# Kernel optimization log

Measured on AMD Instinct MI355X. Metric: run time of the kernel, lower is better.

The kernel has to match this reference:

```python
import jax, jax.numpy as jnp
import numpy as np

L, B, S, D, H, FF = 6, 4, 1024, 256, 8, 128
DH = D // H
EPS = 1e-5


def _ln(x, w, b):
    m = x.mean(-1, keepdims=True)
    v = ((x - m) ** 2).mean(-1, keepdims=True)
    return (x - m) / jnp.sqrt(v + EPS) * w + b


def setup_inputs() -> dict:
    key = jax.random.key(0)
    ks = jax.random.split(key, 6)
    s = lambda k, shape: jax.random.normal(k, shape, jnp.float32) * 0.02
    return {
        "x": jax.random.normal(ks[0], (B, S, D), jnp.float32),
        "ln1_w": jnp.ones((L, D), jnp.float32),
        "ln1_b": jnp.zeros((L, D), jnp.float32),
        "wqkv": s(ks[1], (L, D, 3 * D)),   # qkv_linear, bias=False
        "wout": s(ks[2], (L, D, D)),       # out_linear, bias=False
        "ln2_w": jnp.ones((L, D), jnp.float32),
        "ln2_b": jnp.zeros((L, D), jnp.float32),
        "w1": s(ks[3], (L, D, 2 * FF)),    # Linear(d_model, 2*ff)
        "b1": jnp.zeros((L, 2 * FF), jnp.float32),
        "w2": s(ks[4], (L, FF, D)),        # Linear(ff, d_model)
        "b2": jnp.zeros((L, D), jnp.float32),
    }


def reference(x, ln1_w, ln1_b, wqkv, wout, ln2_w, ln2_b, w1, b1, w2, b2):
    attn_weights_list = []
    scale = 1.0 / jnp.sqrt(jnp.float32(DH))
    for i in range(L):
        # --- pre-norm multi-head attention ---
        xn = _ln(x, ln1_w[i], ln1_b[i])
        qkv = xn @ wqkv[i]                       # [B,S,3D]
        q, k, v = jnp.split(qkv, 3, axis=-1)
        rs = lambda t: t.reshape(B, S, H, DH).transpose(0, 2, 1, 3)  # b h s d
        q, k, v = rs(q), rs(k), rs(v)
        logits = jnp.einsum('bhid,bhjd->bhij', q, k) * scale
        aw = jax.nn.softmax(logits, axis=-1)     # [B,H,S,S] (dropout=0, eval)
        attn_weights_list.append(aw)
        o = jnp.einsum('bhij,bhjd->bhid', aw, v)
        o = o.transpose(0, 2, 1, 3).reshape(B, S, D) @ wout[i]
        x = x + o
        # --- pre-norm GEGLU FFN ---
        h = _ln(x, ln2_w[i], ln2_b[i]) @ w1[i] + b1[i]   # [B,S,2*FF]
        a, g = jnp.split(h, 2, axis=-1)
        x = x + (a * jax.nn.gelu(g, approximate=False)) @ w2[i] + b2[i]
    return x, jnp.stack(attn_weights_list)      # [B,S,D], [L,B,H,S,S]
```

## Files before the change

### kernel.cpp

```cpp
#include <hip/hip_runtime.h>
#include <hip/hip_bf16.h>

typedef __bf16 bf16x8 __attribute__((ext_vector_type(8)));
typedef __bf16 bf16x4 __attribute__((ext_vector_type(4)));
typedef __bf16 bf16x2 __attribute__((ext_vector_type(2)));
typedef float  f32x4  __attribute__((ext_vector_type(4)));

#define LAYERS 6
#define BATCH  4
#define SEQ    1024
#define DMODEL 256
#define NHEAD  8
#define DHEAD  32
#define FFDIM  128
#define ROWS   (BATCH*SEQ)
#define QKVN   (3*DMODEL)
#define QSCALE 0.2550348616f

static __device__ __forceinline__ bf16x8 ldg8(const __bf16* p) {
  return *reinterpret_cast<const bf16x8*>(p);
}
#define MFMA16(a, b, c) __builtin_amdgcn_mfma_f32_16x16x32_bf16((a), (b), (c), 0, 0, 0)

__global__ void k_prep(const float* __restrict__ wqkv, const float* __restrict__ wout,
                       const float* __restrict__ w1, const float* __restrict__ w2,
                       __bf16* __restrict__ wqkvT, __bf16* __restrict__ woutT,
                       __bf16* __restrict__ w1T, __bf16* __restrict__ w2T) {
  const int N1 = LAYERS * DMODEL * QKVN;
  const int N2 = LAYERS * DMODEL * DMODEL;
  const int N3 = LAYERS * DMODEL * 2 * FFDIM;
  const int N4 = LAYERS * FFDIM * DMODEL;
  int total = N1 + N2 + N3 + N4;
  for (int i = blockIdx.x * blockDim.x + threadIdx.x; i < total; i += gridDim.x * blockDim.x) {
    int j = i;
    if (j < N1) {
      int l = j / (DMODEL * QKVN), rc = j - l * (DMODEL * QKVN);
      int r = rc / QKVN, c = rc - r * QKVN;
      wqkvT[(size_t)l * DMODEL * QKVN + (size_t)c * DMODEL + r] = (__bf16)wqkv[j]; continue;
    } j -= N1;
    if (j < N2) {
      int l = j / (DMODEL * DMODEL), rc = j - l * (DMODEL * DMODEL);
      int r = rc / DMODEL, c = rc - r * DMODEL;
      woutT[(size_t)l * DMODEL * DMODEL + (size_t)c * DMODEL + r] = (__bf16)wout[j]; continue;
    } j -= N2;
    if (j < N3) {
      int l = j / (DMODEL * 2 * FFDIM), rc = j - l * (DMODEL * 2 * FFDIM);
      int r = rc / (2 * FFDIM), c = rc - r * (2 * FFDIM);
      w1T[(size_t)l * DMODEL * 2 * FFDIM + (size_t)c * DMODEL + r] = (__bf16)w1[j]; continue;
    } j -= N3;
    {
      int l = j / (FFDIM * DMODEL), rc = j - l * (FFDIM * DMODEL);
      int r = rc / DMODEL, c = rc - r * DMODEL;
      w2T[(size_t)l * FFDIM * DMODEL + (size_t)c * FFDIM + r] = (__bf16)w2[j];
    }
  }
}

__global__ __launch_bounds__(64) void k_ln(const float* __restrict__ x,
                                           const float* __restrict__ w,
                                           const float* __restrict__ b,
                                           __bf16* __restrict__ out) {
  int row = blockIdx.x, l = threadIdx.x;
  const float* xr = x + (size_t)row * DMODEL;
  float v[4];
  #pragma unroll
  for (int j = 0; j < 4; ++j) v[j] = xr[l + 64 * j];
  float s = v[0] + v[1] + v[2] + v[3];
  #pragma unroll
  for (int off = 32; off >= 1; off >>= 1) s += __shfl_xor(s, off);
  float mean = s * (1.0f / DMODEL);
  float sq = 0.f;
  #pragma unroll
  for (int j = 0; j < 4; ++j) { v[j] -= mean; sq += v[j] * v[j]; }
  #pragma unroll
  for (int off = 32; off >= 1; off >>= 1) sq += __shfl_xor(sq, off);
  float rstd = rsqrtf(sq * (1.0f / DMODEL) + 1e-5f);
  __bf16* orow = out + (size_t)row * DMODEL;
  #pragma unroll
  for (int j = 0; j < 4; ++j) {
    int c = l + 64 * j;
    orow[c] = (__bf16)(v[j] * rstd * w[c] + b[c]);
  }
}

__global__ __launch_bounds__(256) void k_qkv(const __bf16* __restrict__ xn,
                                             const __bf16* __restrict__ Bt,
                                             __bf16* __restrict__ qb,
                                             __bf16* __restrict__ kt,
                                             __bf16* __restrict__ vt) {
  int w = threadIdx.x >> 6, l = threadIdx.x & 63, lr = l & 15, lg = l >> 4;
  int m0 = blockIdx.x * 64 + w * 16;
  int n0 = blockIdx.y * 64;
  f32x4 acc[4] = {};
  const __bf16* ap = xn + (size_t)(m0 + lr) * DMODEL + 8 * lg;
  const __bf16* bp = Bt + (size_t)(n0 + lr) * DMODEL + 8 * lg;
  for (int kc = 0; kc < DMODEL; kc += 32) {
    bf16x8 a = ldg8(ap + kc);
    #pragma unroll
    for (int t = 0; t < 4; ++t) {
      bf16x8 b = ldg8(bp + (size_t)t * 16 * DMODEL + kc);
      acc[t] = MFMA16(a, b, acc[t]);
    }
  }
  int row = m0 + lg * 4;
  if (n0 < DMODEL) {
    #pragma unroll
    for (int t = 0; t < 4; ++t) {
      int col = n0 + t * 16 + lr;
      #pragma unroll
      for (int r = 0; r < 4; ++r)
        qb[(size_t)(row + r) * DMODEL + col] = (__bf16)(acc[t][r] * QSCALE);
    }
  } else if (n0 < 2 * DMODEL) {
    int b_ = row >> 10, s = row & (SEQ - 1);
    #pragma unroll
    for (int t = 0; t < 4; ++t) {
      int hdh = n0 - DMODEL + t * 16 + lr;
      int h = hdh >> 5, dh = hdh & 31;
      size_t base = ((size_t)(b_ * NHEAD + h) * SEQ + s) * DHEAD + dh;
      #pragma unroll
      for (int r = 0; r < 4; ++r) kt[base + (size_t)r * DHEAD] = (__bf16)acc[t][r];
    }
  } else {
    int b_ = row >> 10, s = row & (SEQ - 1);
    #pragma unroll
    for (int t = 0; t < 4; ++t) {
      int hdh = n0 - 2 * DMODEL + t * 16 + lr;
      int h = hdh >> 5, dh = hdh & 31;
      bf16x4 v4;
      #pragma unroll
      for (int r = 0; r < 4; ++r) v4[r] = (__bf16)acc[t][r];
      *reinterpret_cast<bf16x4*>(vt + ((size_t)(b_ * NHEAD + h) * DHEAD + dh) * SEQ + s) = v4;
    }
  }
}

__global__ __launch_bounds__(256, 4) void k_attn(const __bf16* __restrict__ qb,
                                                 const __bf16* __restrict__ kt,
                                                 const __bf16* __restrict__ vt,
                                                 __bf16* __restrict__ ob,
                                                 float* __restrict__ aw) {
  __shared__ __bf16 P[4][2][16][40];
  __shared__ float  Ssum[4][16];
  __shared__ float  OS[4][16][34];
  int h = blockIdx.y, b = blockIdx.z;
  int w = threadIdx.x >> 6, l = threadIdx.x & 63, lr = l & 15, lg = l >> 4;
  int q0 = blockIdx.x * 16;
  bf16x8 qf = ldg8(qb + ((size_t)(b * SEQ) + q0 + lr) * DMODEL + h * DHEAD + 8 * lg);
  const __bf16* ktb = kt + (size_t)(b * NHEAD + h) * SEQ * DHEAD + 8 * lg;
  const __bf16* vtb = vt + (size_t)(b * NHEAD + h) * DHEAD * SEQ;
  f32x4 z = {};
  int kbeg = w * 256;

  f32x4 p[16];
  f32x4 accO[2] = {};

  #pragma unroll
  for (int j = 0; j < 8; ++j) {
    int kc = kbeg + j * 32;
    #pragma unroll
    for (int half = 0; half < 2; ++half) {
      int t = j * 2 + half;
      bf16x8 kf = ldg8(ktb + (size_t)(kc + half * 16 + lr) * DHEAD);
      f32x4 d = MFMA16(qf, kf, z);
      #pragma unroll
      for (int r = 0; r < 4; ++r) {
        p[t][r] = exp2f(d[r]);
        P[w][j & 1][lg * 4 + r][half * 16 + lr] = (__bf16)p[t][r];
      }
    }
    if (j > 0) {
      bf16x8 pf  = *reinterpret_cast<const bf16x8*>(&P[w][(j & 1) ^ 1][lr][8 * lg]);
      bf16x8 vf0 = ldg8(vtb + (size_t)lr * SEQ + (kc - 32) + 8 * lg);
      bf16x8 vf1 = ldg8(vtb + (size_t)(16 + lr) * SEQ + (kc - 32) + 8 * lg);
      accO[0] = MFMA16(pf, vf0, accO[0]);
      accO[1] = MFMA16(pf, vf1, accO[1]);
    }
  }
  {
    bf16x8 pf  = *reinterpret_cast<const bf16x8*>(&P[w][1][lr][8 * lg]);
    bf16x8 vf0 = ldg8(vtb + (size_t)lr * SEQ + (kbeg + 224) + 8 * lg);
    bf16x8 vf1 = ldg8(vtb + (size_t)(16 + lr) * SEQ + (kbeg + 224) + 8 * lg);
    accO[0] = MFMA16(pf, vf0, accO[0]);
    accO[1] = MFMA16(pf, vf1, accO[1]);
  }

  float s4[4] = {0.f, 0.f, 0.f, 0.f};
  #pragma unroll
  for (int t = 0; t < 16; ++t)
    #pragma unroll
    for (int r = 0; r < 4; ++r) s4[r] += p[t][r];
  #pragma unroll
  for (int off = 1; off < 16; off <<= 1) {
    #pragma unroll
    for (int r = 0; r < 4; ++r) s4[r] += __shfl_xor(s4[r], off);
  }
  if (lr == 0) {
    #pragma unroll
    for (int r = 0; r < 4; ++r) Ssum[w][lg * 4 + r] = s4[r];
  }
  __syncthreads();
  float rinv[4];
  #pragma unroll
  for (int r = 0; r < 4; ++r) {
    int row = lg * 4 + r;
    rinv[r] = 1.0f / (Ssum[0][row] + Ssum[1][row] + Ssum[2][row] + Ssum[3][row]);
  }

  float* awb = aw + ((size_t)(b * NHEAD + h) * SEQ) * SEQ;
  #pragma unroll
  for (int t = 0; t < 16; ++t) {
    int k0 = kbeg + t * 16;
    #pragma unroll
    for (int r = 0; r < 4; ++r)
      __builtin_nontemporal_store(p[t][r] * rinv[r],
                                  &awb[(size_t)(q0 + lg * 4 + r) * SEQ + k0 + lr]);
  }

  #pragma unroll
  for (int t = 0; t < 2; ++t)
    #pragma unroll
    for (int r = 0; r < 4; ++r) OS[w][lg * 4 + r][t * 16 + lr] = accO[t][r] * rinv[r];
  __syncthreads();
  int idx = threadIdx.x * 2;
  int row = idx >> 5, col = idx & 31;
  float o0 = OS[0][row][col] + OS[1][row][col] + OS[2][row][col] + OS[3][row][col];
  float o1 = OS[0][row][col + 1] + OS[1][row][col + 1] + OS[2][row][col + 1] + OS[3][row][col + 1];
  bf16x2 o2; o2[0] = (__bf16)o0; o2[1] = (__bf16)o1;
  *reinterpret_cast<bf16x2*>(ob + ((size_t)(b * SEQ) + q0 + row) * DMODEL + h * DHEAD + col) = o2;
}

template <int LAST>
__global__ __launch_bounds__(256) void k_pf(const __bf16* __restrict__ ob,
                                            const __bf16* __restrict__ woutT,
                                            const float* __restrict__ xres,
                                            const float* __restrict__ ln2w,
                                            const float* __restrict__ ln2b,
                                            const __bf16* __restrict__ w1t,
                                            const float* __restrict__ b1,
                                            const __bf16* __restrict__ w2t,
                                            const float* __restrict__ b2,
                                            float* __restrict__ x32out,
                                            const float* __restrict__ lnw_n,
                                            const float* __restrict__ lnb_n,
                                            __bf16* __restrict__ xn_next,
                                            float* __restrict__ xout) {
  __shared__ float  xs[16][268];
  __shared__ __bf16 XN[16][264];
  __shared__ __bf16 G[16][136];
  __shared__ __bf16 HT[16][136];
  int w = threadIdx.x >> 6, l = threadIdx.x & 63, lr = l & 15, lg = l >> 4;
  int m0 = blockIdx.x * 16;
  int n0 = w * 64;
  {
    f32x4 acc[4] = {};
    const __bf16* ap = ob + (size_t)(m0 + lr) * DMODEL + 8 * lg;
    const __bf16* bp = woutT + (size_t)(n0 + lr) * DMODEL + 8 * lg;
    for (int kc = 0; kc < DMODEL; kc += 32) {
      bf16x8 a = ldg8(ap + kc);
      #pragma unroll
      for (int t = 0; t < 4; ++t) {
        bf16x8 b = ldg8(bp + (size_t)t * 16 * DMODEL + kc);
        acc[t] = MFMA16(a, b, acc[t]);
      }
    }
    #pragma unroll
    for (int t = 0; t < 4; ++t) {
      int col = n0 + t * 16 + lr;
      #pragma unroll
      for (int r = 0; r < 4; ++r) {
        int row = lg * 4 + r;
        xs[row][col] = acc[t][r] + xres[(size_t)(m0 + row) * DMODEL + col];
      }
    }
  }
  __syncthreads();
  #pragma unroll
  for (int rr = 0; rr < 4; ++rr) {
    int row = w * 4 + rr;
    f32x4 v = *reinterpret_cast<const f32x4*>(&xs[row][4 * l]);
    float s = v[0] + v[1] + v[2] + v[3];
    #pragma unroll
    for (int off = 32; off >= 1; off >>= 1) s += __shfl_xor(s, off);
    float mean = s * (1.0f / DMODEL);
    float sq = 0.f;
    f32x4 c;
    #pragma unroll
    for (int j = 0; j < 4; ++j) { c[j] = v[j] - mean; sq += c[j] * c[j]; }
    #pragma unroll
    for (int off = 32; off >= 1; off >>= 1) sq += __shfl_xor(sq, off);
    float rstd = rsqrtf(sq * (1.0f / DMODEL) + 1e-5f);
    f32x4 lwv = *reinterpret_cast<const f32x4*>(&ln2w[4 * l]);
    f32x4 lbv = *reinterpret_cast<const f32x4*>(&ln2b[4 * l]);
    bf16x4 o4;
    #pragma unroll
    for (int j = 0; j < 4; ++j) o4[j] = (__bf16)(c[j] * rstd * lwv[j] + lbv[j]);
    *reinterpret_cast<bf16x4*>(&XN[row][4 * l]) = o4;
  }
  __syncthreads();
  f32x4 acc1[4] = {};
  {
    const __bf16* bp = w1t + (size_t)(n0 + lr) * DMODEL + 8 * lg;
    for (int kc = 0; kc < DMODEL; kc += 32) {
      bf16x8 a = *reinterpret_cast<const bf16x8*>(&XN[lr][kc + 8 * lg]);
      #pragma unroll
      for (int t = 0; t < 4; ++t) {
        bf16x8 bfr = ldg8(bp + (size_t)t * 16 * DMODEL + kc);
        acc1[t] = MFMA16(a, bfr, acc1[t]);
      }
    }
  }
  if (w >= 2) {
    #pragma unroll
    for (int t = 0; t < 4; ++t) {
      int col = n0 + t * 16 + lr;
      #pragma unroll
      for (int r = 0; r < 4; ++r) {
        float g = acc1[t][r] + b1[col];
        float ge = 0.5f * g * (1.0f + erff(g * 0.70710678118654752f));
        G[lg * 4 + r][col - 128] = (__bf16)ge;
      }
    }
  }
  __syncthreads();
  if (w < 2) {
    #pragma unroll
    for (int t = 0; t < 4; ++t) {
      int col = n0 + t * 16 + lr;
      #pragma unroll
      for (int r = 0; r < 4; ++r) {
        float a1 = acc1[t][r] + b1[col];
        HT[lg * 4 + r][col] = (__bf16)(a1 * (float)G[lg * 4 + r][col]);
      }
    }
  }
  __syncthreads();
  {
    f32x4 acc2[4] = {};
    const __bf16* bp = w2t + (size_t)(n0 + lr) * FFDIM + 8 * lg;
    for (int kc = 0; kc < FFDIM; kc += 32) {
      bf16x8 a2 = *reinterpret_cast<const bf16x8*>(&HT[lr][kc + 8 * lg]);
      #pragma unroll
      for (int t = 0; t < 4; ++t) {
        bf16x8 bfr = ldg8(bp + (size_t)t * 16 * FFDIM + kc);
        acc2[t] = MFMA16(a2, bfr, acc2[t]);
      }
    }
    #pragma unroll
    for (int t = 0; t < 4; ++t) {
      int col = n0 + t * 16 + lr;
      #pragma unroll
      for (int r = 0; r < 4; ++r) {
        int row = lg * 4 + r;
        xs[row][col] = acc2[t][r] + b2[col] + xs[row][col];
      }
    }
  }
  __syncthreads();
  #pragma unroll
  for (int rr = 0; rr < 4; ++rr) {
    int row = w * 4 + rr;
    f32x4 v = *reinterpret_cast<const f32x4*>(&xs[row][4 * l]);
    if (LAST) {
      *reinterpret_cast<f32x4*>(&xout[(size_t)(m0 + row) * DMODEL + 4 * l]) = v;
    } else {
      float s = v[0] + v[1] + v[2] + v[3];
      #pragma unroll
      for (int off = 32; off >= 1; off >>= 1) s += __shfl_xor(s, off);
      float mean = s * (1.0f / DMODEL);
      float sq = 0.f;
      f32x4 c;
      #pragma unroll
      for (int j = 0; j < 4; ++j) { c[j] = v[j] - mean; sq += c[j] * c[j]; }
      #pragma unroll
      for (int off = 32; off >= 1; off >>= 1) sq += __shfl_xor(sq, off);
      float rstd = rsqrtf(sq * (1.0f / DMODEL) + 1e-5f);
      *reinterpret_cast<f32x4*>(&x32out[(size_t)(m0 + row) * DMODEL + 4 * l]) = v;
      f32x4 lwv = *reinterpret_cast<const f32x4*>(&lnw_n[4 * l]);
      f32x4 lbv = *reinterpret_cast<const f32x4*>(&lnb_n[4 * l]);
      bf16x4 o4;
      #pragma unroll
      for (int j = 0; j < 4; ++j) o4[j] = (__bf16)(c[j] * rstd * lwv[j] + lbv[j]);
      *reinterpret_cast<bf16x4*>(&xn_next[(size_t)(m0 + row) * DMODEL + 4 * l]) = o4;
    }
  }
}

static inline size_t align256(size_t x) { return (x + 255) & ~(size_t)255; }

extern "C" void kernel_launch(void* const* d_in, const int* in_sizes, int n_in,
                              void* d_out, int out_size, void* d_ws, size_t ws_size,
                              hipStream_t stream) {
  const float* x_in = (const float*)d_in[0];
  const float* ln1w = (const float*)d_in[1];
  const float* ln1b = (const float*)d_in[2];
  const float* wqkv = (const float*)d_in[3];
  const float* wout = (const float*)d_in[4];
  const float* ln2w = (const float*)d_in[5];
  const float* ln2b = (const float*)d_in[6];
  const float* w1   = (const float*)d_in[7];
  const float* b1   = (const float*)d_in[8];
  const float* w2   = (const float*)d_in[9];
  const float* b2   = (const float*)d_in[10];
  float* out = (float*)d_out;

  char* p = (char*)d_ws;
  float*  x32   = (float*)p;  p += align256((size_t)ROWS * DMODEL * 4);
  __bf16* xn    = (__bf16*)p; p += align256((size_t)ROWS * DMODEL * 2);
  __bf16* qb    = (__bf16*)p; p += align256((size_t)ROWS * DMODEL * 2);
  __bf16* kt    = (__bf16*)p; p += align256((size_t)ROWS * DMODEL * 2);
  __bf16* vt    = (__bf16*)p; p += align256((size_t)ROWS * DMODEL * 2);
  __bf16* ob    = (__bf16*)p; p += align256((size_t)ROWS * DMODEL * 2);
  __bf16* wqkvT = (__bf16*)p; p += align256((size_t)LAYERS * DMODEL * QKVN * 2);
  __bf16* woutT = (__bf16*)p; p += align256((size_t)LAYERS * DMODEL * DMODEL * 2);
  __bf16* w1T   = (__bf16*)p; p += align256((size_t)LAYERS * DMODEL * 2 * FFDIM * 2);
  __bf16* w2T   = (__bf16*)p; p += align256((size_t)LAYERS * FFDIM * DMODEL * 2);

  k_prep<<<2048, 256, 0, stream>>>(wqkv, wout, w1, w2, wqkvT, woutT, w1T, w2T);
  k_ln<<<ROWS, 64, 0, stream>>>(x_in, ln1w, ln1b, xn);

  const size_t AW_LAYER = (size_t)BATCH * NHEAD * SEQ * SEQ;
  for (int i = 0; i < LAYERS; ++i) {
    k_qkv<<<dim3(ROWS / 64, QKVN / 64), 256, 0, stream>>>(
        xn, wqkvT + (size_t)i * DMODEL * QKVN, qb, kt, vt);
    float* aw_l = out + (size_t)ROWS * DMODEL + (size_t)i * AW_LAYER;
    k_attn<<<dim3(SEQ / 16, NHEAD, BATCH), 256, 0, stream>>>(qb, kt, vt, ob, aw_l);
    const float* xres = (i == 0) ? x_in : x32;
    if (i < LAYERS - 1) {
      k_pf<0><<<ROWS / 16, 256, 0, stream>>>(
          ob, woutT + (size_t)i * DMODEL * DMODEL, xres,
          ln2w + i * DMODEL, ln2b + i * DMODEL,
          w1T + (size_t)i * DMODEL * 2 * FFDIM, b1 + i * 2 * FFDIM,
          w2T + (size_t)i * FFDIM * DMODEL, b2 + i * DMODEL,
          x32, ln1w + (i + 1) * DMODEL, ln1b + (i + 1) * DMODEL, xn, nullptr);
    } else {
      k_pf<1><<<ROWS / 16, 256, 0, stream>>>(
          ob, woutT + (size_t)i * DMODEL * DMODEL, xres,
          ln2w + i * DMODEL, ln2b + i * DMODEL,
          w1T + (size_t)i * DMODEL * 2 * FFDIM, b1 + i * 2 * FFDIM,
          w2T + (size_t)i * FFDIM * DMODEL, b2 + i * DMODEL,
          x32, nullptr, nullptr, nullptr, out);
    }
  }
}
```

Baseline: 507.0 us.

## Fuse next-layer QKV projection into post-attention FFN kernel and swizzle attention grid

The post-attention/FFN kernel now runs 512 threads per 16-row tile and, for non-final layers, computes the next layer's QKV projection directly from the LayerNorm output held in shared memory. This removes the separate k_qkv launch for later layers and the write and re-read of the normalized activations through global memory. The attention kernel uses a 1D grid with a swizzled block index that reorders which (query block, head, batch) tiles run together, likely aiming at better cache locality for K/V. The fused QKV step reloads the full QKV weight slice in every 16-row block, which adds weight traffic and work to an already long kernel.

```diff
diff --git a/kernel.cpp b/kernel.cpp
--- a/kernel.cpp
+++ b/kernel.cpp
@@ -143,9 +143,11 @@
   __shared__ __bf16 P[4][2][16][40];
   __shared__ float  Ssum[4][16];
   __shared__ float  OS[4][16][34];
-  int h = blockIdx.y, b = blockIdx.z;
+  int bid = blockIdx.x;
+  int swz = (bid & 7) * 256 + (bid >> 3);
+  int qblk = swz & 63, h = (swz >> 6) & 7, b = swz >> 9;
   int w = threadIdx.x >> 6, l = threadIdx.x & 63, lr = l & 15, lg = l >> 4;
-  int q0 = blockIdx.x * 16;
+  int q0 = qblk * 16;
   bf16x8 qf = ldg8(qb + ((size_t)(b * SEQ) + q0 + lr) * DMODEL + h * DHEAD + 8 * lg);
   const __bf16* ktb = kt + (size_t)(b * NHEAD + h) * SEQ * DHEAD + 8 * lg;
   const __bf16* vtb = vt + (size_t)(b * NHEAD + h) * DHEAD * SEQ;
@@ -231,7 +233,7 @@
 }
 
 template <int LAST>
-__global__ __launch_bounds__(256) void k_pf(const __bf16* __restrict__ ob,
+__global__ __launch_bounds__(512) void k_pf(const __bf16* __restrict__ ob,
                                             const __bf16* __restrict__ woutT,
                                             const float* __restrict__ xres,
                                             const float* __restrict__ ln2w,
@@ -243,7 +245,10 @@
                                             float* __restrict__ x32out,
                                             const float* __restrict__ lnw_n,
                                             const float* __restrict__ lnb_n,
-                                            __bf16* __restrict__ xn_next,
+                                            const __bf16* __restrict__ wqkvT_n,
+                                            __bf16* __restrict__ qb,
+                                            __bf16* __restrict__ kt,
+                                            __bf16* __restrict__ vt,
                                             float* __restrict__ xout) {
   __shared__ float  xs[16][268];
   __shared__ __bf16 XN[16][264];
@@ -251,21 +256,19 @@
   __shared__ __bf16 HT[16][136];
   int w = threadIdx.x >> 6, l = threadIdx.x & 63, lr = l & 15, lg = l >> 4;
   int m0 = blockIdx.x * 16;
-  int n0 = w * 64;
   {
-    f32x4 acc[4] = {};
+    int n0 = w * 32;
+    f32x4 acc[2] = {};
     const __bf16* ap = ob + (size_t)(m0 + lr) * DMODEL + 8 * lg;
     const __bf16* bp = woutT + (size_t)(n0 + lr) * DMODEL + 8 * lg;
     for (int kc = 0; kc < DMODEL; kc += 32) {
       bf16x8 a = ldg8(ap + kc);
       #pragma unroll
-      for (int t = 0; t < 4; ++t) {
-        bf16x8 b = ldg8(bp + (size_t)t * 16 * DMODEL + kc);
-        acc[t] = MFMA16(a, b, acc[t]);
-      }
-    }
-    #pragma unroll
-    for (int t = 0; t < 4; ++t) {
+      for (int t = 0; t < 2; ++t)
+        acc[t] = MFMA16(a, ldg8(bp + (size_t)t * 16 * DMODEL + kc), acc[t]);
+    }
+    #pragma unroll
+    for (int t = 0; t < 2; ++t) {
       int col = n0 + t * 16 + lr;
       #pragma unroll
       for (int r = 0; r < 4; ++r) {
@@ -276,8 +279,8 @@
   }
   __syncthreads();
   #pragma unroll
-  for (int rr = 0; rr < 4; ++rr) {
-    int row = w * 4 + rr;
+  for (int rr = 0; rr < 2; ++rr) {
+    int row = w * 2 + rr;
     f32x4 v = *reinterpret_cast<const f32x4*>(&xs[row][4 * l]);
     float s = v[0] + v[1] + v[2] + v[3];
     #pragma unroll
@@ -298,22 +301,21 @@
     *reinterpret_cast<bf16x4*>(&XN[row][4 * l]) = o4;
   }
   __syncthreads();
-  f32x4 acc1[4] = {};
+  int n0f = w * 32;
+  f32x4 acc1[2] = {};
   {
-    const __bf16* bp = w1t + (size_t)(n0 + lr) * DMODEL + 8 * lg;
+    const __bf16* bp = w1t + (size_t)(n0f + lr) * DMODEL + 8 * lg;
     for (int kc = 0; kc < DMODEL; kc += 32) {
       bf16x8 a = *reinterpret_cast<const bf16x8*>(&XN[lr][kc + 8 * lg]);
       #pragma unroll
-      for (int t = 0; t < 4; ++t) {
-        bf16x8 bfr = ldg8(bp + (size_t)t * 16 * DMODEL + kc);
-        acc1[t] = MFMA16(a, bfr, acc1[t]);
-      }
-    }
-  }
-  if (w >= 2) {
-    #pragma unroll
-    for (int t = 0; t < 4; ++t) {
-      int col = n0 + t * 16 + lr;
+      for (int t = 0; t < 2; ++t)
+        acc1[t] = MFMA16(a, ldg8(bp + (size_t)t * 16 * DMODEL + kc), acc1[t]);
+    }
+  }
+  if (w >= 4) {
+    #pragma unroll
+    for (int t = 0; t < 2; ++t) {
+      int col = n0f + t * 16 + lr;
       #pragma unroll
       for (int r = 0; r < 4; ++r) {
         float g = acc1[t][r] + b1[col];
@@ -323,10 +325,10 @@
     }
   }
   __syncthreads();
-  if (w < 2) {
-    #pragma unroll
-    for (int t = 0; t < 4; ++t) {
-      int col = n0 + t * 16 + lr;
+  if (w < 4) {
+    #pragma unroll
+    for (int t = 0; t < 2; ++t) {
+      int col = n0f + t * 16 + lr;
       #pragma unroll
       for (int r = 0; r < 4; ++r) {
         float a1 = acc1[t][r] + b1[col];
@@ -336,19 +338,17 @@
   }
   __syncthreads();
   {
-    f32x4 acc2[4] = {};
-    const __bf16* bp = w2t + (size_t)(n0 + lr) * FFDIM + 8 * lg;
+    f32x4 acc2[2] = {};
+    const __bf16* bp = w2t + (size_t)(n0f + lr) * FFDIM + 8 * lg;
     for (int kc = 0; kc < FFDIM; kc += 32) {
       bf16x8 a2 = *reinterpret_cast<const bf16x8*>(&HT[lr][kc + 8 * lg]);
       #pragma unroll
-      for (int t = 0; t < 4; ++t) {
-        bf16x8 bfr = ldg8(bp + (size_t)t * 16 * FFDIM + kc);
-        acc2[t] = MFMA16(a2, bfr, acc2[t]);
-      }
-    }
-    #pragma unroll
-    for (int t = 0; t < 4; ++t) {
-      int col = n0 + t * 16 + lr;
+      for (int t = 0; t < 2; ++t)
+        acc2[t] = MFMA16(a2, ldg8(bp + (size_t)t * 16 * FFDIM + kc), acc2[t]);
+    }
+    #pragma unroll
+    for (int t = 0; t < 2; ++t) {
+      int col = n0f + t * 16 + lr;
       #pragma unroll
       for (int r = 0; r < 4; ++r) {
         int row = lg * 4 + r;
@@ -358,8 +358,8 @@
   }
   __syncthreads();
   #pragma unroll
-  for (int rr = 0; rr < 4; ++rr) {
-    int row = w * 4 + rr;
+  for (int rr = 0; rr < 2; ++rr) {
+    int row = w * 2 + rr;
     f32x4 v = *reinterpret_cast<const f32x4*>(&xs[row][4 * l]);
     if (LAST) {
       *reinterpret_cast<f32x4*>(&xout[(size_t)(m0 + row) * DMODEL + 4 * l]) = v;
@@ -381,7 +381,44 @@
       bf16x4 o4;
       #pragma unroll
       for (int j = 0; j < 4; ++j) o4[j] = (__bf16)(c[j] * rstd * lwv[j] + lbv[j]);
-      *reinterpret_cast<bf16x4*>(&xn_next[(size_t)(m0 + row) * DMODEL + 4 * l]) = o4;
+      *reinterpret_cast<bf16x4*>(&XN[row][4 * l]) = o4;
+    }
+  }
+  if (!LAST) {
+    __syncthreads();
+    f32x4 acc[6] = {};
+    {
+      const __bf16* bp = wqkvT_n + (size_t)(w * 96 + lr) * DMODEL + 8 * lg;
+      for (int kc = 0; kc < DMODEL; kc += 32) {
+        bf16x8 a = *reinterpret_cast<const bf16x8*>(&XN[lr][kc + 8 * lg]);
+        #pragma unroll
+        for (int t = 0; t < 6; ++t)
+          acc[t] = MFMA16(a, ldg8(bp + (size_t)t * 16 * DMODEL + kc), acc[t]);
+      }
+    }
+    int row = m0 + lg * 4;
+    int b_ = row >> 10, s = row & (SEQ - 1);
+    #pragma unroll
+    for (int t = 0; t < 6; ++t) {
+      int col = w * 96 + t * 16 + lr;
+      if (col < DMODEL) {
+        #pragma unroll
+        for (int r = 0; r < 4; ++r)
+          qb[(size_t)(row + r) * DMODEL + col] = (__bf16)(acc[t][r] * QSCALE);
+      } else if (col < 2 * DMODEL) {
+        int hdh = col - DMODEL;
+        int h = hdh >> 5, dh = hdh & 31;
+        size_t base = ((size_t)(b_ * NHEAD + h) * SEQ + s) * DHEAD + dh;
+        #pragma unroll
+        for (int r = 0; r < 4; ++r) kt[base + (size_t)r * DHEAD] = (__bf16)acc[t][r];
+      } else {
+        int hdh = col - 2 * DMODEL;
+        int h = hdh >> 5, dh = hdh & 31;
+        bf16x4 v4;
+        #pragma unroll
+        for (int r = 0; r < 4; ++r) v4[r] = (__bf16)acc[t][r];
+        *reinterpret_cast<bf16x4*>(vt + ((size_t)(b_ * NHEAD + h) * DHEAD + dh) * SEQ + s) = v4;
+      }
     }
   }
 }
@@ -418,28 +455,28 @@
 
   k_prep<<<2048, 256, 0, stream>>>(wqkv, wout, w1, w2, wqkvT, woutT, w1T, w2T);
   k_ln<<<ROWS, 64, 0, stream>>>(x_in, ln1w, ln1b, xn);
+  k_qkv<<<dim3(ROWS / 64, QKVN / 64), 256, 0, stream>>>(xn, wqkvT, qb, kt, vt);
 
   const size_t AW_LAYER = (size_t)BATCH * NHEAD * SEQ * SEQ;
   for (int i = 0; i < LAYERS; ++i) {
-    k_qkv<<<dim3(ROWS / 64, QKVN / 64), 256, 0, stream>>>(
-        xn, wqkvT + (size_t)i * DMODEL * QKVN, qb, kt, vt);
     float* aw_l = out + (size_t)ROWS * DMODEL + (size_t)i * AW_LAYER;
-    k_attn<<<dim3(SEQ / 16, NHEAD, BATCH), 256, 0, stream>>>(qb, kt, vt, ob, aw_l);
+    k_attn<<<SEQ / 16 * NHEAD * BATCH, 256, 0, stream>>>(qb, kt, vt, ob, aw_l);
     const float* xres = (i == 0) ? x_in : x32;
     if (i < LAYERS - 1) {
-      k_pf<0><<<ROWS / 16, 256, 0, stream>>>(
+      k_pf<0><<<ROWS / 16, 512, 0, stream>>>(
           ob, woutT + (size_t)i * DMODEL * DMODEL, xres,
           ln2w + i * DMODEL, ln2b + i * DMODEL,
           w1T + (size_t)i * DMODEL * 2 * FFDIM, b1 + i * 2 * FFDIM,
           w2T + (size_t)i * FFDIM * DMODEL, b2 + i * DMODEL,
-          x32, ln1w + (i + 1) * DMODEL, ln1b + (i + 1) * DMODEL, xn, nullptr);
+          x32, ln1w + (i + 1) * DMODEL, ln1b + (i + 1) * DMODEL,
+          wqkvT + (size_t)(i + 1) * DMODEL * QKVN, qb, kt, vt, nullptr);
     } else {
-      k_pf<1><<<ROWS / 16, 256, 0, stream>>>(
+      k_pf<1><<<ROWS / 16, 512, 0, stream>>>(
           ob, woutT + (size_t)i * DMODEL * DMODEL, xres,
           ln2w + i * DMODEL, ln2b + i * DMODEL,
           w1T + (size_t)i * DMODEL * 2 * FFDIM, b1 + i * 2 * FFDIM,
           w2T + (size_t)i * FFDIM * DMODEL, b2 + i * DMODEL,
-          x32, nullptr, nullptr, nullptr, out);
-    }
-  }
-}
+          x32, nullptr, nullptr, nullptr, nullptr, nullptr, nullptr, out);
+    }
+  }
+}
```

Result: faster. 493.0 us (-2.8%).
